# Kernel tuning notes

Hardware: AMD Instinct MI355X
Metric: run time of the kernel (lower is better)

The kernel has to match this reference:

```python
import jax, jax.numpy as jnp
import numpy as np

B, F, H, E, V, T = 128, 2048, 1024, 512, 16384, 20
TEMP = 1.0


def setup_inputs() -> dict:
    key = jax.random.key(0)
    ks = jax.random.split(key, 12)
    sc = lambda i, shape, s=0.02: jax.random.normal(ks[i], shape, jnp.float32) * s
    # Gumbel(0,1) noise for RelaxedOneHotCategorical.rsample
    u = jax.random.uniform(ks[11], (T, B, V), jnp.float32, 1e-6, 1.0 - 1e-6)
    gumbel = -jnp.log(-jnp.log(u))
    return dict(
        image_features=jax.random.normal(ks[0], (B, F), jnp.float32),
        agent_w=sc(1, (H, F)),
        agent_b=jnp.zeros((H,), jnp.float32),
        w_ih=sc(2, (3 * H, E)),
        w_hh=sc(3, (3 * H, H)),
        b_ih=jnp.zeros((3 * H,), jnp.float32),
        b_hh=jnp.zeros((3 * H,), jnp.float32),
        w_out=sc(4, (V, H)),
        b_out=jnp.zeros((V,), jnp.float32),
        emb_w=sc(5, (E, V)),
        sos=sc(6, (E,), 0.01),
        gumbel=gumbel,
    )


def _gru_cell(x, h, w_ih, w_hh, b_ih, b_hh):
    # torch.nn.GRUCell math
    gi = x @ w_ih.T + b_ih          # [B, 3H]
    gh = h @ w_hh.T + b_hh          # [B, 3H]
    i_r, i_z, i_n = jnp.split(gi, 3, axis=-1)
    h_r, h_z, h_n = jnp.split(gh, 3, axis=-1)
    r = jax.nn.sigmoid(i_r + h_r)
    z = jax.nn.sigmoid(i_z + h_z)
    n = jnp.tanh(i_n + r * h_n)
    return (1.0 - z) * n + z * h


def reference(image_features, agent_w, agent_b, w_ih, w_hh, b_ih, b_hh,
              w_out, b_out, emb_w, sos, gumbel):
    h0 = image_features @ agent_w.T + agent_b                 # agent: [B, H]
    e0 = jnp.broadcast_to(sos, (image_features.shape[0], sos.shape[0]))  # SOS embed

    def step(carry, g_t):
        h, e = carry
        h = _gru_cell(e, h, w_ih, w_hh, b_ih, b_hh)            # [B, H]
        logits = h @ w_out.T + b_out                           # [B, V]
        # Gumbel-softmax sample (training mode, not straight-through)
        x = jax.nn.softmax((logits + g_t) / TEMP, axis=-1)     # [B, V]
        e = x @ emb_w.T                                        # soft-one-hot embedding, [B, E]
        return (h, e), x

    _, seq = jax.lax.scan(step, (h0, e0), gumbel)              # [T, B, V]
    return jnp.transpose(seq, (1, 0, 2))                       # [B, T, V]
```

## Files before the change

### kernel.cpp

```cpp
#include <hip/hip_runtime.h>
#include <hip/hip_bf16.h>
#include <math.h>

namespace {

constexpr int kB = 128, kF = 2048, kH = 1024, kE = 512, kV = 16384, kT = 20;

typedef __attribute__((ext_vector_type(4))) float f32x4;
typedef __attribute__((ext_vector_type(8))) short bf16x8;

#define MFMA(a, b, c) __builtin_amdgcn_mfma_f32_16x16x32_bf16((a), (b), (c), 0, 0, 0)

__device__ __forceinline__ short f2bf(float f) {
  union { float f; unsigned u; } un;
  un.f = f;
  unsigned x = un.u;
  x += 0x7fffu + ((x >> 16) & 1u);
  return (short)(x >> 16);
}

__device__ __forceinline__ float bf2f(short s) {
  union { unsigned u; float f; } un;
  un.u = ((unsigned)(unsigned short)s) << 16;
  return un.f;
}

__device__ __forceinline__ float sigm(float x) { return 1.0f / (1.0f + __expf(-x)); }

__device__ __forceinline__ void cvt4(const float* __restrict__ s, short* __restrict__ d,
                                     long n4, long gid, long gs) {
  for (long i = gid; i < n4; i += gs) {
    float4 v = ((const float4*)s)[i];
    short4 o;
    o.x = f2bf(v.x); o.y = f2bf(v.y); o.z = f2bf(v.z); o.w = f2bf(v.w);
    ((short4*)d)[i] = o;
  }
}

__global__ __launch_bounds__(256) void k_convert(
    const float* __restrict__ wout, const float* __restrict__ emb,
    const float* __restrict__ wih, const float* __restrict__ whh,
    const float* __restrict__ aw, const float* __restrict__ img,
    const float* __restrict__ sos,
    short* __restrict__ wout_b, short* __restrict__ emb_b,
    short* __restrict__ wih_b, short* __restrict__ whh_b,
    short* __restrict__ aw_b, short* __restrict__ img_b,
    float* __restrict__ e_f) {
  long gid = (long)blockIdx.x * blockDim.x + threadIdx.x;
  long gs = (long)gridDim.x * blockDim.x;
  cvt4(wout, wout_b, (long)kV * kH / 4, gid, gs);
  cvt4(emb, emb_b, (long)kE * kV / 4, gid, gs);
  cvt4(wih, wih_b, (long)3 * kH * kE / 4, gid, gs);
  cvt4(whh, whh_b, (long)3 * kH * kH / 4, gid, gs);
  cvt4(aw, aw_b, (long)kH * kF / 4, gid, gs);
  cvt4(img, img_b, (long)kB * kF / 4, gid, gs);
  for (long i = gid; i < kB * kE; i += gs) e_f[i] = sos[i & (kE - 1)];
}

__global__ __launch_bounds__(256) void k_h0(const short* __restrict__ img_b,
                                            const short* __restrict__ aw_b,
                                            const float* __restrict__ ab,
                                            float* __restrict__ hf, short* __restrict__ hb) {
  int tid = threadIdx.x;
  int l = tid & 63, w = tid >> 6;
  int lr = l & 15, g = l >> 4, lk = g * 8;
  int col0 = blockIdx.x * 16;
  int row0 = w * 32;
  f32x4 acc[2] = {};
#pragma unroll 4
  for (int k0 = 0; k0 < kF; k0 += 32) {
    bf16x8 a0 = *(const bf16x8*)&img_b[(row0 + lr) * kF + k0 + lk];
    bf16x8 a1 = *(const bf16x8*)&img_b[(row0 + 16 + lr) * kF + k0 + lk];
    bf16x8 b = *(const bf16x8*)&aw_b[(size_t)(col0 + lr) * kF + k0 + lk];
    acc[0] = MFMA(a0, b, acc[0]);
    acc[1] = MFMA(a1, b, acc[1]);
  }
  int col = col0 + lr;
  float bias = ab[col];
#pragma unroll
  for (int mf = 0; mf < 2; ++mf)
#pragma unroll
    for (int j = 0; j < 4; ++j) {
      int row = row0 + mf * 16 + g * 4 + j;
      float v = acc[mf][j] + bias;
      hf[row * kH + col] = v;
      hb[row * kH + col] = f2bf(v);
    }
}

__global__ __launch_bounds__(512) void k_gru(
    const float* __restrict__ e_f, const short* __restrict__ hb_prev,
    float* __restrict__ hf,
    const short* __restrict__ wih_b, const short* __restrict__ whh_b,
    const float* __restrict__ bih, const float* __restrict__ bhh,
    short* __restrict__ hb_next, float* __restrict__ denom_cur,
    const short* __restrict__ p_prev, const float* __restrict__ denom_prev,
    float* __restrict__ out_prev) {
  int tid = threadIdx.x, bid = blockIdx.x;
  int l = tid & 63, w = tid >> 6;
  int lr = l & 15, g = l >> 4, lk = g * 8;
  __shared__ f32x4 part[4][2][2][64];
  int colt = bid >> 2, rq = bid & 3;
  int col0 = colt * 16;
  if (w < 4) {
    int rh = w & 1, kq = w >> 1;
    int row0 = rq * 32 + rh * 16;
    if (bid == 0 && tid < 32) {
      f32x4 z = {0.0f, 0.0f, 0.0f, 0.0f};
      *(f32x4*)&denom_cur[tid * 4] = z;
    }
    f32x4 ar = {}, az = {}, ain = {}, ahn = {};
    if (kq == 0) {
#pragma unroll 4
      for (int ki = 0; ki < 16; ++ki) {
        int k0 = ki * 32;
        float4 af0 = *(const float4*)&e_f[(row0 + lr) * kE + k0 + lk];
        float4 af1 = *(const float4*)&e_f[(row0 + lr) * kE + k0 + lk + 4];
        bf16x8 a;
        a[0] = f2bf(af0.x); a[1] = f2bf(af0.y); a[2] = f2bf(af0.z); a[3] = f2bf(af0.w);
        a[4] = f2bf(af1.x); a[5] = f2bf(af1.y); a[6] = f2bf(af1.z); a[7] = f2bf(af1.w);
        bf16x8 br = *(const bf16x8*)&wih_b[(size_t)(col0 + lr) * kE + k0 + lk];
        bf16x8 bz = *(const bf16x8*)&wih_b[(size_t)(kH + col0 + lr) * kE + k0 + lk];
        bf16x8 bn = *(const bf16x8*)&wih_b[(size_t)(2 * kH + col0 + lr) * kE + k0 + lk];
        ar = MFMA(a, br, ar);
        az = MFMA(a, bz, az);
        ain = MFMA(a, bn, ain);
      }
#pragma unroll 4
      for (int ki = 0; ki < 8; ++ki) {
        int k0 = ki * 32;
        bf16x8 a = *(const bf16x8*)&hb_prev[(row0 + lr) * kH + k0 + lk];
        bf16x8 br = *(const bf16x8*)&whh_b[(size_t)(col0 + lr) * kH + k0 + lk];
        bf16x8 bz = *(const bf16x8*)&whh_b[(size_t)(kH + col0 + lr) * kH + k0 + lk];
        bf16x8 bn = *(const bf16x8*)&whh_b[(size_t)(2 * kH + col0 + lr) * kH + k0 + lk];
        ar = MFMA(a, br, ar);
        az = MFMA(a, bz, az);
        ahn = MFMA(a, bn, ahn);
      }
    } else {
#pragma unroll 4
      for (int ki = 0; ki < 24; ++ki) {
        int k0 = 256 + ki * 32;
        bf16x8 a = *(const bf16x8*)&hb_prev[(row0 + lr) * kH + k0 + lk];
        bf16x8 br = *(const bf16x8*)&whh_b[(size_t)(col0 + lr) * kH + k0 + lk];
        bf16x8 bz = *(const bf16x8*)&whh_b[(size_t)(kH + col0 + lr) * kH + k0 + lk];
        bf16x8 bn = *(const bf16x8*)&whh_b[(size_t)(2 * kH + col0 + lr) * kH + k0 + lk];
        ar = MFMA(a, br, ar);
        az = MFMA(a, bz, az);
        ahn = MFMA(a, bn, ahn);
      }
    }
    part[0][rh][kq][l] = ar;
    part[1][rh][kq][l] = az;
    part[2][rh][kq][l] = ain;
    part[3][rh][kq][l] = ahn;
  } else if (out_prev != nullptr) {
    int r = bid >> 1, halfc = bid & 1;
    float rd = 1.0f / denom_prev[r];
    int coff = halfc * 8192 + (w - 4) * 2048 + l * 32;
    const short* pr = p_prev + (size_t)r * kV + coff;
    float* orow = out_prev + (size_t)r * (kT * kV) + coff;
#pragma unroll
    for (int jj = 0; jj < 4; ++jj) {
      bf16x8 p8 = *(const bf16x8*)(pr + jj * 8);
      f32x4 o0, o1;
      o0[0] = bf2f(p8[0]) * rd; o0[1] = bf2f(p8[1]) * rd;
      o0[2] = bf2f(p8[2]) * rd; o0[3] = bf2f(p8[3]) * rd;
      o1[0] = bf2f(p8[4]) * rd; o1[1] = bf2f(p8[5]) * rd;
      o1[2] = bf2f(p8[6]) * rd; o1[3] = bf2f(p8[7]) * rd;
      __builtin_nontemporal_store(o0, (f32x4*)(orow + jj * 8));
      __builtin_nontemporal_store(o1, (f32x4*)(orow + jj * 8 + 4));
    }
  }
  __syncthreads();
  if (w < 2) {
    int rh2 = w;
    int row0e = rq * 32 + rh2 * 16;
    f32x4 rs = part[0][rh2][0][l] + part[0][rh2][1][l];
    f32x4 zs = part[1][rh2][0][l] + part[1][rh2][1][l];
    f32x4 is = part[2][rh2][0][l] + part[2][rh2][1][l];
    f32x4 hs = part[3][rh2][0][l] + part[3][rh2][1][l];
    int col = col0 + lr;
    float bihr = bih[col], bhhr = bhh[col];
    float bihz = bih[kH + col], bhhz = bhh[kH + col];
    float bihn = bih[2 * kH + col], bhhn = bhh[2 * kH + col];
#pragma unroll
    for (int j = 0; j < 4; ++j) {
      int row = row0e + g * 4 + j;
      float r = sigm(rs[j] + bihr + bhhr);
      float z = sigm(zs[j] + bihz + bhhz);
      float nn = tanhf(is[j] + bihn + r * (hs[j] + bhhn));
      float hv = (1.0f - z) * nn + z * hf[row * kH + col];
      hf[row * kH + col] = hv;
      hb_next[row * kH + col] = f2bf(hv);
    }
  }
}

__global__ __launch_bounds__(256, 2) void k_logits(
    const short* __restrict__ h_b, const short* __restrict__ wout_b,
    const float* __restrict__ bout, const float* __restrict__ gum_t,
    short* __restrict__ p_b, float* __restrict__ denom, float* __restrict__ e_f) {
  __shared__ char lds[32 * 2064];
  __shared__ float ls[2][2][64];
  int tid = threadIdx.x;
  int l = tid & 63, w = tid >> 6;
  int lr = l & 15, g = l >> 4, lk = g * 8;
  int wm = w & 1, wn = w >> 1;
  int col = blockIdx.x * 32 + wn * 16 + lr;
  int mrow0 = wm * 64;
  int gi = blockIdx.x * 256 + tid;
  if (gi < kB * kE) e_f[gi] = 0.0f;
  float gmr[16];
#pragma unroll
  for (int mf = 0; mf < 4; ++mf)
#pragma unroll
    for (int j = 0; j < 4; ++j)
      gmr[mf * 4 + j] = __builtin_nontemporal_load(
          &gum_t[(size_t)(mrow0 + mf * 16 + g * 4 + j) * kV + col]);
  float bo = bout[col];
  {
    const char* src = (const char*)(wout_b + (size_t)blockIdx.x * 32 * kH);
#pragma unroll
    for (int i = 0; i < 16; ++i) {
      int c = tid + i * 256;
      int row = c >> 7;
      int within = (c & 127) * 16;
      bf16x8 v = *(const bf16x8*)(src + c * 16);
      *(bf16x8*)(&lds[row * 2064 + within]) = v;
    }
  }
  __syncthreads();
  const char* bbase = &lds[(wn * 16 + lr) * 2064 + lk * 2];
  f32x4 acc[4] = {};
  bf16x8 arg[2][4];
#pragma unroll
  for (int k = 0; k < 2; ++k)
#pragma unroll
    for (int mf = 0; mf < 4; ++mf)
      arg[k][mf] = *(const bf16x8*)&h_b[(mrow0 + mf * 16 + lr) * kH + k * 32 + lk];
#pragma unroll
  for (int k = 0; k < 32; ++k) {
    bf16x8 b = *(const bf16x8*)(bbase + k * 64);
    acc[0] = MFMA(arg[k & 1][0], b, acc[0]);
    acc[1] = MFMA(arg[k & 1][1], b, acc[1]);
    acc[2] = MFMA(arg[k & 1][2], b, acc[2]);
    acc[3] = MFMA(arg[k & 1][3], b, acc[3]);
    if (k < 30) {
#pragma unroll
      for (int mf = 0; mf < 4; ++mf)
        arg[k & 1][mf] =
            *(const bf16x8*)&h_b[(mrow0 + mf * 16 + lr) * kH + (k + 2) * 32 + lk];
    }
  }
  float p[16];
#pragma unroll
  for (int i = 0; i < 16; ++i) p[i] = __expf(acc[i >> 2][i & 3] + bo + gmr[i]);
#pragma unroll
  for (int i = 0; i < 16; ++i) {
    int rl = (i >> 2) * 16 + g * 4 + (i & 3);
    p_b[(size_t)(mrow0 + rl) * kV + col] = f2bf(p[i]);
  }
#pragma unroll
  for (int i = 0; i < 16; ++i) {
    float s = p[i];
#pragma unroll
    for (int sf = 1; sf < 16; sf <<= 1) s += __shfl_xor(s, sf, 64);
    if (lr == 0) ls[wm][wn][(i >> 2) * 16 + g * 4 + (i & 3)] = s;
  }
  __syncthreads();
  if (tid < 128) {
    int row = tid;
    float sb = ls[row >> 6][0][row & 63] + ls[row >> 6][1][row & 63];
    atomicAdd(&denom[row], sb);
  }
}

__global__ __launch_bounds__(512) void k_e(
    const short* __restrict__ p_b, const float* __restrict__ denom,
    const short* __restrict__ emb_b, float* __restrict__ e_f) {
  int tid = threadIdx.x;
  int l = tid & 63, w = tid >> 6;
  int lr = l & 15, g = l >> 4, lk = g * 8;
  int wm = w >> 2, wn = w & 3;
  int kc = blockIdx.x >> 3, et = blockIdx.x & 7;
  int kbase = kc * 512;
  int colB = et * 64 + wn * 16 + lr;
  __shared__ float s_rd[kB];
  if (tid < kB) s_rd[tid] = 1.0f / denom[tid];
  __shared__ bf16x8 xs8[2048];
  char* xs = (char*)xs8;
  int colg = tid & 15, rrow = tid >> 4;
  f32x4 acc[4] = {};
  __syncthreads();
  for (int s = 0; s < 4; ++s) {
    if (s) __syncthreads();
#pragma unroll
    for (int rr = 0; rr < 4; ++rr) {
      int row = rr * 32 + rrow;
      int cb = s * 128 + colg * 8;
      bf16x8 p8 = *(const bf16x8*)&p_b[(size_t)row * kV + kbase + cb];
      float scl = s_rd[row];
      bf16x8 xv;
#pragma unroll
      for (int i = 0; i < 8; ++i) xv[i] = f2bf(bf2f(p8[i]) * scl);
      unsigned off = (unsigned)(row * 256 + colg * 16) ^ ((row & 7) << 4);
      *(bf16x8*)(xs + off) = xv;
    }
    __syncthreads();
#pragma unroll
    for (int kk = 0; kk < 4; ++kk) {
      bf16x8 b = *(const bf16x8*)&emb_b[(size_t)colB * kV + kbase + s * 128 + kk * 32 + lk];
#pragma unroll
      for (int mf = 0; mf < 4; ++mf) {
        int rowa = wm * 64 + mf * 16 + lr;
        unsigned off = (unsigned)(rowa * 256 + (kk * 32 + lk) * 2) ^ ((rowa & 7) << 4);
        bf16x8 a = *(const bf16x8*)(xs + off);
        acc[mf] = MFMA(a, b, acc[mf]);
      }
    }
  }
#pragma unroll
  for (int mf = 0; mf < 4; ++mf)
#pragma unroll
    for (int j = 0; j < 4; ++j) {
      int row = wm * 64 + mf * 16 + g * 4 + j;
      atomicAdd(&e_f[row * kE + et * 64 + wn * 16 + lr], acc[mf][j]);
    }
}

__global__ __launch_bounds__(256) void k_out(const short* __restrict__ p_b,
                                             const float* __restrict__ denom,
                                             float* __restrict__ outp) {
  int tid = threadIdx.x, bid = blockIdx.x;
  int r = bid >> 1, halfc = bid & 1;
  float rd = 1.0f / denom[r];
  int coff = halfc * 8192 + tid * 32;
  const short* pr = p_b + (size_t)r * kV + coff;
  float* orow = outp + (size_t)r * (kT * kV) + coff;
#pragma unroll
  for (int jj = 0; jj < 4; ++jj) {
    bf16x8 p8 = *(const bf16x8*)(pr + jj * 8);
    f32x4 o0, o1;
    o0[0] = bf2f(p8[0]) * rd; o0[1] = bf2f(p8[1]) * rd;
    o0[2] = bf2f(p8[2]) * rd; o0[3] = bf2f(p8[3]) * rd;
    o1[0] = bf2f(p8[4]) * rd; o1[1] = bf2f(p8[5]) * rd;
    o1[2] = bf2f(p8[6]) * rd; o1[3] = bf2f(p8[7]) * rd;
    __builtin_nontemporal_store(o0, (f32x4*)(orow + jj * 8));
    __builtin_nontemporal_store(o1, (f32x4*)(orow + jj * 8 + 4));
  }
}

}

extern "C" void kernel_launch(void* const* d_in, const int* in_sizes, int n_in,
                              void* d_out, int out_size, void* d_ws, size_t ws_size,
                              hipStream_t stream) {
  const float* img = (const float*)d_in[0];
  const float* aw = (const float*)d_in[1];
  const float* ab = (const float*)d_in[2];
  const float* wih = (const float*)d_in[3];
  const float* whh = (const float*)d_in[4];
  const float* bih = (const float*)d_in[5];
  const float* bhh = (const float*)d_in[6];
  const float* wout = (const float*)d_in[7];
  const float* bout = (const float*)d_in[8];
  const float* emb = (const float*)d_in[9];
  const float* sos = (const float*)d_in[10];
  const float* gum = (const float*)d_in[11];
  float* out = (float*)d_out;
  char* ws = (char*)d_ws;

  short* wout_b = (short*)(ws + 0);
  short* emb_b = (short*)(ws + 33554432);
  short* wih_b = (short*)(ws + 50331648);
  short* whh_b = (short*)(ws + 53477376);
  short* aw_b = (short*)(ws + 59768832);
  short* img_b = (short*)(ws + 63963136);
  float* hf = (float*)(ws + 64487424);
  short* hb0 = (short*)(ws + 65011712);
  short* hb1 = (short*)(ws + 65273856);
  short* p_b = (short*)(ws + 65536000);
  float* denoms = (float*)(ws + 69730304);
  float* e_f = (float*)(ws + 69732352);

  short* hb[2] = {hb0, hb1};

  k_convert<<<2048, 256, 0, stream>>>(wout, emb, wih, whh, aw, img, sos, wout_b, emb_b,
                                      wih_b, whh_b, aw_b, img_b, e_f);
  k_h0<<<64, 256, 0, stream>>>(img_b, aw_b, ab, hf, hb[0]);
  for (int t = 0; t < kT; ++t) {
    int rp = t & 1, wp = rp ^ 1;
    float* denomC = denoms + (t & 1) * 256;
    float* denomP = denoms + ((t & 1) ^ 1) * 256;
    float* out_prev = (t == 0) ? nullptr : out + (size_t)(t - 1) * kV;
    k_gru<<<256, 512, 0, stream>>>(e_f, hb[rp], hf, wih_b, whh_b, bih, bhh, hb[wp],
                                   denomC, p_b, denomP, out_prev);
    k_logits<<<512, 256, 0, stream>>>(hb[wp], wout_b, bout, gum + (size_t)t * kB * kV,
                                      p_b, denomC, e_f);
    k_e<<<256, 512, 0, stream>>>(p_b, denomC, emb_b, e_f);
  }
  k_out<<<256, 256, 0, stream>>>(p_b, denoms + 256, out + (size_t)(kT - 1) * kV);
}
```

Measured before the change: 1.935 ms.

## Double-buffer weight loads in GRU kernel and prefetch emb/p tiles in k_e

In the GRU gate kernel, the weight fragments for W_ih and W_hh are now register double-buffered, loaded two k-steps ahead, and the loops are fully unrolled so global-load latency overlaps the MFMAs. In k_e, the embedding tile is staged into a padded LDS double buffer, and the next stage's probability and embedding tiles are prefetched into registers while the current stage's MFMAs run. The aim is to hide memory latency in both latency-bound inner loops. The cost is higher register pressure and more LDS use in k_e, which could lower occupancy.

```diff
diff --git a/kernel.cpp b/kernel.cpp
--- a/kernel.cpp
+++ b/kernel.cpp
@@ -110,8 +110,21 @@
       *(f32x4*)&denom_cur[tid * 4] = z;
     }
     f32x4 ar = {}, az = {}, ain = {}, ahn = {};
+    const short* wrp = &wih_b[(size_t)(col0 + lr) * kE + lk];
+    const short* wzp = &wih_b[(size_t)(kH + col0 + lr) * kE + lk];
+    const short* wnp = &wih_b[(size_t)(2 * kH + col0 + lr) * kE + lk];
+    const short* hrp = &whh_b[(size_t)(col0 + lr) * kH + lk];
+    const short* hzp = &whh_b[(size_t)(kH + col0 + lr) * kH + lk];
+    const short* hnp = &whh_b[(size_t)(2 * kH + col0 + lr) * kH + lk];
     if (kq == 0) {
-#pragma unroll 4
+      bf16x8 rr[2], rz[2], rn[2];
+#pragma unroll
+      for (int k = 0; k < 2; ++k) {
+        rr[k] = *(const bf16x8*)(wrp + k * 32);
+        rz[k] = *(const bf16x8*)(wzp + k * 32);
+        rn[k] = *(const bf16x8*)(wnp + k * 32);
+      }
+#pragma unroll
       for (int ki = 0; ki < 16; ++ki) {
         int k0 = ki * 32;
         float4 af0 = *(const float4*)&e_f[(row0 + lr) * kE + k0 + lk];
@@ -119,35 +132,55 @@
         bf16x8 a;
         a[0] = f2bf(af0.x); a[1] = f2bf(af0.y); a[2] = f2bf(af0.z); a[3] = f2bf(af0.w);
         a[4] = f2bf(af1.x); a[5] = f2bf(af1.y); a[6] = f2bf(af1.z); a[7] = f2bf(af1.w);
-        bf16x8 br = *(const bf16x8*)&wih_b[(size_t)(col0 + lr) * kE + k0 + lk];
-        bf16x8 bz = *(const bf16x8*)&wih_b[(size_t)(kH + col0 + lr) * kE + k0 + lk];
-        bf16x8 bn = *(const bf16x8*)&wih_b[(size_t)(2 * kH + col0 + lr) * kE + k0 + lk];
-        ar = MFMA(a, br, ar);
-        az = MFMA(a, bz, az);
-        ain = MFMA(a, bn, ain);
-      }
-#pragma unroll 4
+        ar = MFMA(a, rr[ki & 1], ar);
+        az = MFMA(a, rz[ki & 1], az);
+        ain = MFMA(a, rn[ki & 1], ain);
+        if (ki < 14) {
+          rr[ki & 1] = *(const bf16x8*)(wrp + (ki + 2) * 32);
+          rz[ki & 1] = *(const bf16x8*)(wzp + (ki + 2) * 32);
+          rn[ki & 1] = *(const bf16x8*)(wnp + (ki + 2) * 32);
+        }
+      }
+      bf16x8 hr[2], hz[2], hn[2];
+#pragma unroll
+      for (int k = 0; k < 2; ++k) {
+        hr[k] = *(const bf16x8*)(hrp + k * 32);
+        hz[k] = *(const bf16x8*)(hzp + k * 32);
+        hn[k] = *(const bf16x8*)(hnp + k * 32);
+      }
+#pragma unroll
       for (int ki = 0; ki < 8; ++ki) {
         int k0 = ki * 32;
         bf16x8 a = *(const bf16x8*)&hb_prev[(row0 + lr) * kH + k0 + lk];
-        bf16x8 br = *(const bf16x8*)&whh_b[(size_t)(col0 + lr) * kH + k0 + lk];
-        bf16x8 bz = *(const bf16x8*)&whh_b[(size_t)(kH + col0 + lr) * kH + k0 + lk];
-        bf16x8 bn = *(const bf16x8*)&whh_b[(size_t)(2 * kH + col0 + lr) * kH + k0 + lk];
-        ar = MFMA(a, br, ar);
-        az = MFMA(a, bz, az);
-        ahn = MFMA(a, bn, ahn);
+        ar = MFMA(a, hr[ki & 1], ar);
+        az = MFMA(a, hz[ki & 1], az);
+        ahn = MFMA(a, hn[ki & 1], ahn);
+        if (ki < 6) {
+          hr[ki & 1] = *(const bf16x8*)(hrp + (ki + 2) * 32);
+          hz[ki & 1] = *(const bf16x8*)(hzp + (ki + 2) * 32);
+          hn[ki & 1] = *(const bf16x8*)(hnp + (ki + 2) * 32);
+        }
       }
     } else {
-#pragma unroll 4
+      bf16x8 hr[2], hz[2], hn[2];
+#pragma unroll
+      for (int k = 0; k < 2; ++k) {
+        hr[k] = *(const bf16x8*)(hrp + (8 + k) * 32);
+        hz[k] = *(const bf16x8*)(hzp + (8 + k) * 32);
+        hn[k] = *(const bf16x8*)(hnp + (8 + k) * 32);
+      }
+#pragma unroll
       for (int ki = 0; ki < 24; ++ki) {
         int k0 = 256 + ki * 32;
         bf16x8 a = *(const bf16x8*)&hb_prev[(row0 + lr) * kH + k0 + lk];
-        bf16x8 br = *(const bf16x8*)&whh_b[(size_t)(col0 + lr) * kH + k0 + lk];
-        bf16x8 bz = *(const bf16x8*)&whh_b[(size_t)(kH + col0 + lr) * kH + k0 + lk];
-        bf16x8 bn = *(const bf16x8*)&whh_b[(size_t)(2 * kH + col0 + lr) * kH + k0 + lk];
-        ar = MFMA(a, br, ar);
-        az = MFMA(a, bz, az);
-        ahn = MFMA(a, bn, ahn);
+        ar = MFMA(a, hr[ki & 1], ar);
+        az = MFMA(a, hz[ki & 1], az);
+        ahn = MFMA(a, hn[ki & 1], ahn);
+        if (ki < 22) {
+          hr[ki & 1] = *(const bf16x8*)(hrp + (ki + 10) * 32);
+          hz[ki & 1] = *(const bf16x8*)(hzp + (ki + 10) * 32);
+          hn[ki & 1] = *(const bf16x8*)(hnp + (ki + 10) * 32);
+        }
       }
     }
     part[0][rh][kq][l] = ar;
@@ -285,21 +318,27 @@
   int wm = w >> 2, wn = w & 3;
   int kc = blockIdx.x >> 3, et = blockIdx.x & 7;
   int kbase = kc * 512;
-  int colB = et * 64 + wn * 16 + lr;
   __shared__ float s_rd[kB];
+  __shared__ bf16x8 xs8[2048];
+  __shared__ char es[2][64 * 264];
+  char* xs = (char*)xs8;
   if (tid < kB) s_rd[tid] = 1.0f / denom[tid];
-  __shared__ bf16x8 xs8[2048];
-  char* xs = (char*)xs8;
+  __syncthreads();
   int colg = tid & 15, rrow = tid >> 4;
-  f32x4 acc[4] = {};
-  __syncthreads();
-  for (int s = 0; s < 4; ++s) {
-    if (s) __syncthreads();
+  int ec0 = tid * 2, ec1 = tid * 2 + 1;
+  int er0 = ec0 >> 4, ew0 = (ec0 & 15) * 16;
+  int er1 = ec1 >> 4, ew1 = (ec1 & 15) * 16;
+  const char* esrc0 = (const char*)&emb_b[(size_t)(et * 64 + er0) * kV + kbase] + ew0;
+  const char* esrc1 = (const char*)&emb_b[(size_t)(et * 64 + er1) * kV + kbase] + ew1;
+  {
+    bf16x8 e0 = *(const bf16x8*)esrc0;
+    bf16x8 e1 = *(const bf16x8*)esrc1;
+    *(bf16x8*)&es[0][er0 * 264 + ew0] = e0;
+    *(bf16x8*)&es[0][er1 * 264 + ew1] = e1;
 #pragma unroll
     for (int rr = 0; rr < 4; ++rr) {
       int row = rr * 32 + rrow;
-      int cb = s * 128 + colg * 8;
-      bf16x8 p8 = *(const bf16x8*)&p_b[(size_t)row * kV + kbase + cb];
+      bf16x8 p8 = *(const bf16x8*)&p_b[(size_t)row * kV + kbase + colg * 8];
       float scl = s_rd[row];
       bf16x8 xv;
 #pragma unroll
@@ -307,10 +346,25 @@
       unsigned off = (unsigned)(row * 256 + colg * 16) ^ ((row & 7) << 4);
       *(bf16x8*)(xs + off) = xv;
     }
-    __syncthreads();
+  }
+  __syncthreads();
+  f32x4 acc[4] = {};
+  int ebrow = wn * 16 + lr;
+  for (int s = 0; s < 4; ++s) {
+    int cur = s & 1;
+    bf16x8 ne0, ne1, np[4];
+    if (s < 3) {
+      ne0 = *(const bf16x8*)(esrc0 + (s + 1) * 256);
+      ne1 = *(const bf16x8*)(esrc1 + (s + 1) * 256);
+#pragma unroll
+      for (int rr = 0; rr < 4; ++rr) {
+        int row = rr * 32 + rrow;
+        np[rr] = *(const bf16x8*)&p_b[(size_t)row * kV + kbase + (s + 1) * 128 + colg * 8];
+      }
+    }
 #pragma unroll
     for (int kk = 0; kk < 4; ++kk) {
-      bf16x8 b = *(const bf16x8*)&emb_b[(size_t)colB * kV + kbase + s * 128 + kk * 32 + lk];
+      bf16x8 b = *(const bf16x8*)&es[cur][ebrow * 264 + kk * 64 + lk * 2];
 #pragma unroll
       for (int mf = 0; mf < 4; ++mf) {
         int rowa = wm * 64 + mf * 16 + lr;
@@ -318,6 +372,22 @@
         bf16x8 a = *(const bf16x8*)(xs + off);
         acc[mf] = MFMA(a, b, acc[mf]);
       }
+    }
+    if (s < 3) {
+      __syncthreads();
+      *(bf16x8*)&es[cur ^ 1][er0 * 264 + ew0] = ne0;
+      *(bf16x8*)&es[cur ^ 1][er1 * 264 + ew1] = ne1;
+#pragma unroll
+      for (int rr = 0; rr < 4; ++rr) {
+        int row = rr * 32 + rrow;
+        float scl = s_rd[row];
+        bf16x8 xv;
+#pragma unroll
+        for (int i = 0; i < 8; ++i) xv[i] = f2bf(bf2f(np[rr][i]) * scl);
+        unsigned off = (unsigned)(row * 256 + colg * 16) ^ ((row & 7) << 4);
+        *(bf16x8*)(xs + off) = xv;
+      }
+      __syncthreads();
     }
   }
 #pragma unroll
```

After: 1.822 ms. -5.8%, faster.
